# Kernel tuning notes

Measured on AMD Instinct MI355X. Metric: run time of the kernel, lower is better.

## Reference

```python
import jax, jax.numpy as jnp
import numpy as np

N_NODES = 8192
HIDDEN = 256
HEADS = 4
HEAD_DIM = HIDDEN // HEADS
NUM_EDGES = 4096
NUM_INC = 65536
LN_EPS = 1e-5


def setup_inputs() -> dict:
    key = jax.random.key(0)
    ks = jax.random.split(key, 8)
    scale = HIDDEN ** -0.5
    return {
        "x": jax.random.normal(ks[0], (N_NODES, HIDDEN), jnp.float32),
        "node_idx": jax.random.randint(ks[1], (NUM_INC,), 0, N_NODES),
        "edge_idx": jax.random.randint(ks[2], (NUM_INC,), 0, NUM_EDGES),
        "W_w": jax.random.normal(ks[3], (HIDDEN, HIDDEN), jnp.float32) * scale,
        "W_b": jax.random.normal(ks[4], (HIDDEN,), jnp.float32) * 0.02,
        "edge_att": jax.random.normal(ks[5], (HEADS, HEAD_DIM), jnp.float32) * scale,
        "out_w": jax.random.normal(ks[6], (HIDDEN, HIDDEN), jnp.float32) * scale,
        "out_b": jax.random.normal(ks[7], (HIDDEN,), jnp.float32) * 0.02,
    }


def reference(x, node_idx, edge_idx, W_w, W_b, edge_att, out_w, out_b):
    n = x.shape[0]
    e = node_idx.shape[0]
    # x' = W(x), split into heads: [N, heads, head_dim]
    xw = (x @ W_w.T + W_b).reshape(n, HEADS, HEAD_DIM)
    feat = xw[node_idx]                                   # [E, heads, hd]
    logits = jnp.einsum("ehd,hd->eh", feat, edge_att)      # [E, heads]
    # segment softmax over nodes within each hyperedge, per head
    seg_max = jax.ops.segment_max(logits, edge_idx, num_segments=NUM_EDGES)
    p = jnp.exp(logits - seg_max[edge_idx])
    seg_sum = jax.ops.segment_sum(p, edge_idx, num_segments=NUM_EDGES)
    attn = p / seg_sum[edge_idx]                           # [E, heads]
    attn_mean = attn.mean(axis=1)                          # mean over heads, [E]
    # hyperedges with < 2 nodes are skipped in the original
    sizes = jax.ops.segment_sum(jnp.ones((e,), x.dtype), edge_idx, num_segments=NUM_EDGES)
    valid = sizes[edge_idx] >= 2.0
    attn_mean = jnp.where(valid, attn_mean, 0.0)
    # scatter-add attention-weighted ORIGINAL features back to nodes
    contrib = attn_mean[:, None] * x[node_idx]             # [E, H]
    out = jnp.zeros_like(x).at[node_idx].add(contrib)
    # degree normalization counts ALL incidences (including size-1 edges)
    counts = jnp.zeros((n,), x.dtype).at[node_idx].add(1.0)
    out = out / jnp.clip(counts, 1.0)[:, None]
    out = out @ out_w.T + out_b
    # fresh nn.LayerNorm => affine identity, biased variance, eps=1e-5
    mu = out.mean(-1, keepdims=True)
    var = ((out - mu) ** 2).mean(-1, keepdims=True)
    out = (out - mu) / jnp.sqrt(var + LN_EPS)
    # NxN pairwise attention accumulation: AW[i,j] = sum_e attn_i(e)*count_j(e), diag zeroed
    A = jnp.zeros((n, NUM_EDGES), x.dtype).at[node_idx, edge_idx].add(attn_mean)
    B = jnp.zeros((n, NUM_EDGES), x.dtype).at[node_idx, edge_idx].add(1.0)
    attention_weights = A @ B.T
    attention_weights = attention_weights.at[jnp.diag_indices(n)].set(0.0)
    return out, attention_weights
```

## Files before the change

### kernel.cpp

```cpp
#include <hip/hip_runtime.h>
#include <stdint.h>

#define N_NODES  8192
#define HIDDEN   256
#define HEADS    4
#define HEAD_DIM 64
#define NUM_EDGES 4096
#define NUM_INC  65536
#define LN_EPS   1e-5f

typedef unsigned int uint_t;
typedef float __attribute__((ext_vector_type(4))) f4v;


#define OFF_SEGSZ    0
#define OFF_NCNT     16384
#define OFF_NFILL    49152
#define OFF_EFILL    81920
#define ZERO_BYTES   98304
#define OFF_VKH      98304
#define OFF_BL       102400
#define OFF_LOGIT    102464
#define OFF_NPTR     233536
#define OFF_EPTR     266320
#define OFF_SEGSUM   282720
#define OFF_NINC     348256
#define OFF_EMEM     610400
#define OFF_ITEM     872544

__global__ __launch_bounds__(256) void k_zero(uint_t* __restrict__ w) {
    w[blockIdx.x * 256 + threadIdx.x] = 0u;
}

__global__ __launch_bounds__(256) void k_fold(const float* __restrict__ Ww,
                                              const float* __restrict__ Wb,
                                              const float* __restrict__ ea,
                                              float* __restrict__ vkhT,
                                              float* __restrict__ bl) {
    int k = threadIdx.x, h = blockIdx.x;
    float a = 0.f;
    for (int d = 0; d < HEAD_DIM; ++d)
        a += ea[h * HEAD_DIM + d] * Ww[(size_t)(h * HEAD_DIM + d) * HIDDEN + k];
    vkhT[h * HIDDEN + k] = a;
    if (k == 0) {
        float b = 0.f;
        for (int d = 0; d < HEAD_DIM; ++d)
            b += Wb[h * HEAD_DIM + d] * ea[h * HEAD_DIM + d];
        bl[h] = b;
    }
}

__global__ __launch_bounds__(256) void k_logits(const float* __restrict__ x,
                                                const float* __restrict__ vkhT,
                                                const float* __restrict__ bl,
                                                float* __restrict__ logit) {
    __shared__ __align__(16) float xs[32 * HIDDEN];
    __shared__ __align__(16) float vs[HEADS * HIDDEN];
    __shared__ float bls[HEADS];
    int t = threadIdx.x, b = blockIdx.x;
    float4* xsv = (float4*)xs;
    const float4* xg = (const float4*)(x + (size_t)b * 32 * HIDDEN);
    #pragma unroll
    for (int i = 0; i < 8; ++i) xsv[i * 256 + t] = xg[i * 256 + t];
    ((float4*)vs)[t] = ((const float4*)vkhT)[t];
    if (t < HEADS) bls[t] = bl[t];
    __syncthreads();
    if (t < 128) {
        int n = t >> 2, h = t & 3;
        const float4* xr = (const float4*)(xs + n * HIDDEN);
        const float4* vr = (const float4*)(vs + h * HIDDEN);
        float acc = bls[h];
        for (int k4 = 0; k4 < HIDDEN / 4; ++k4) {
            float4 xv = xr[k4], vv = vr[k4];
            acc += xv.x * vv.x + xv.y * vv.y + xv.z * vv.z + xv.w * vv.w;
        }
        logit[(b * 32 + n) * HEADS + h] = acc;
    }
}

__global__ void k_pass1(const int* __restrict__ node_idx, const int* __restrict__ edge_idx,
                        int* __restrict__ seg_size, int* __restrict__ node_cnt) {
    int i = blockIdx.x * 256 + threadIdx.x;
    atomicAdd(&seg_size[edge_idx[i]], 1);
    atomicAdd(&node_cnt[node_idx[i]], 1);
}

__global__ __launch_bounds__(256) void k_scan(const int* __restrict__ node_cnt, int* __restrict__ node_ptr,
                                              const int* __restrict__ seg_size, int* __restrict__ edge_ptr) {
    __shared__ int part[256];
    const int* cnt; int* ptr; int n;
    if (blockIdx.x == 0) { cnt = node_cnt; ptr = node_ptr; n = N_NODES; }
    else                 { cnt = seg_size; ptr = edge_ptr; n = NUM_EDGES; }
    int t = threadIdx.x, C = n / 256;
    int s = 0;
    for (int j = 0; j < C; ++j) s += cnt[t * C + j];
    part[t] = s;
    __syncthreads();
    if (t == 0) {
        int run = 0;
        for (int i = 0; i < 256; ++i) { int tmp = part[i]; part[i] = run; run += tmp; }
        ptr[n] = run;
    }
    __syncthreads();
    int run = part[t];
    for (int j = 0; j < C; ++j) { ptr[t * C + j] = run; run += cnt[t * C + j]; }
}

__global__ void k_fill(const int* __restrict__ node_idx, const int* __restrict__ edge_idx,
                       const int* __restrict__ node_ptr, const int* __restrict__ edge_ptr,
                       int* __restrict__ node_fill, int* __restrict__ edge_fill,
                       int* __restrict__ node_inc, int* __restrict__ edge_mem) {
    int i = blockIdx.x * 256 + threadIdx.x;
    int n = node_idx[i], e = edge_idx[i];
    int p = node_ptr[n] + atomicAdd(&node_fill[n], 1);
    node_inc[p] = i;
    int q = edge_ptr[e] + atomicAdd(&edge_fill[e], 1);
    edge_mem[q] = n;
}

__global__ __launch_bounds__(256) void k_seg(const int* __restrict__ edge_ptr,
                                             const int* __restrict__ edge_mem,
                                             const float* __restrict__ logit,
                                             float* __restrict__ seg_sum) {
    int e = blockIdx.x * 256 + threadIdx.x;
    int qb = edge_ptr[e], qe = edge_ptr[e + 1];
    float s0 = 0, s1 = 0, s2 = 0, s3 = 0;
    for (int q = qb; q < qe; ++q) {
        int j = edge_mem[q];
        s0 += __expf(logit[j * 4 + 0]);
        s1 += __expf(logit[j * 4 + 1]);
        s2 += __expf(logit[j * 4 + 2]);
        s3 += __expf(logit[j * 4 + 3]);
    }
    seg_sum[e * 4 + 0] = s0; seg_sum[e * 4 + 1] = s1;
    seg_sum[e * 4 + 2] = s2; seg_sum[e * 4 + 3] = s3;
}

__global__ __launch_bounds__(256) void k_pairs(const int* __restrict__ node_inc,
                                               const int* __restrict__ node_idx,
                                               const int* __restrict__ edge_idx,
                                               const int* __restrict__ edge_ptr,
                                               const float* __restrict__ logit,
                                               const float* __restrict__ seg_sum,
                                               float4* __restrict__ item) {
    int p = blockIdx.x * 256 + threadIdx.x;
    int m = node_inc[p];
    int e = edge_idx[m];
    int qb = edge_ptr[e], qe = edge_ptr[e + 1];
    float a = 0.f;
    if (qe - qb >= 2) {
        int n = node_idx[m];
        float s = 0.f;
        #pragma unroll
        for (int h = 0; h < HEADS; ++h)
            s += __expf(logit[n * HEADS + h]) / seg_sum[e * HEADS + h];
        a = 0.25f * s;
    }
    float4 it;
    it.x = a;
    it.y = __int_as_float(qb);
    it.z = __int_as_float(qe);
    it.w = 0.f;
    item[p] = it;
}

__global__ __launch_bounds__(256) void k_out(const float* __restrict__ x,
                                             const int* __restrict__ node_ptr,
                                             const float4* __restrict__ item,
                                             const float* __restrict__ out_w,
                                             const float* __restrict__ out_b,
                                             float* __restrict__ out) {
    __shared__ __align__(16) float y[16][260];
    __shared__ float sr[16], mu_s[16], rs_s[16];
    int t = threadIdx.x;
    int R = blockIdx.x * 16;
    if (t < 16) {
        int n = R + t;
        int pb = node_ptr[n], pe = node_ptr[n + 1];
        float w = 0.f;
        for (int p = pb; p < pe; ++p) w += item[p].x;
        int c = pe - pb; if (c < 1) c = 1;
        sr[t] = w / (float)c;
    }
    __syncthreads();
    #pragma unroll
    for (int r = 0; r < 16; ++r)
        y[r][t] = sr[r] * x[(size_t)(R + r) * HIDDEN + t];
    __syncthreads();
    float acc[16];
    float bias = out_b[t];
    #pragma unroll
    for (int r = 0; r < 16; ++r) acc[r] = bias;
    const float4* wr4 = (const float4*)(out_w + (size_t)t * HIDDEN);
    for (int j4 = 0; j4 < HIDDEN / 4; ++j4) {
        float4 wv = wr4[j4];
        #pragma unroll
        for (int r = 0; r < 16; ++r) {
            float4 yv = *(const float4*)&y[r][j4 * 4];
            acc[r] += yv.x * wv.x + yv.y * wv.y + yv.z * wv.z + yv.w * wv.w;
        }
    }
    __syncthreads();
    #pragma unroll
    for (int r = 0; r < 16; ++r) y[r][t] = acc[r];
    __syncthreads();
    if (t < 16) {
        float m = 0.f;
        for (int j = 0; j < HIDDEN; ++j) m += y[t][j];
        m *= (1.0f / HIDDEN);
        float s2 = 0.f;
        for (int j = 0; j < HIDDEN; ++j) { float d = y[t][j] - m; s2 += d * d; }
        mu_s[t] = m;
        rs_s[t] = rsqrtf(s2 * (1.0f / HIDDEN) + LN_EPS);
    }
    __syncthreads();
    #pragma unroll
    for (int r = 0; r < 16; ++r)
        out[(size_t)(R + r) * HIDDEN + t] = (y[r][t] - mu_s[r]) * rs_s[r];
}

__global__ __launch_bounds__(256) void k_aw(const float4* __restrict__ item,
                                            const int* __restrict__ node_ptr,
                                            const int* __restrict__ edge_mem,
                                            float* __restrict__ AW) {
    __shared__ __align__(16) float row[N_NODES];
    int t = threadIdx.x, w = t >> 6, lane = t & 63;
    int i = blockIdx.x;
    float4* rowv = (float4*)row;
    #pragma unroll
    for (int c = 0; c < 8; ++c) rowv[c * 256 + t] = make_float4(0.f, 0.f, 0.f, 0.f);
    __syncthreads();
    int pb = node_ptr[i], pe = node_ptr[i + 1];
    for (int p = pb + w; p < pe; p += 4) {
        float4 it = item[p];
        float a = it.x;
        if (a != 0.f) {
            int qb = __float_as_int(it.y), qe = __float_as_int(it.z);
            for (int q = qb + lane; q < qe; q += 64)
                atomicAdd(&row[edge_mem[q]], a);
        }
    }
    __syncthreads();
    if (t == 0) row[i] = 0.f;
    __syncthreads();
    f4v* dst = (f4v*)(AW + (size_t)i * N_NODES);
    const f4v* src = (const f4v*)row;
    #pragma unroll
    for (int c = 0; c < 8; ++c)
        __builtin_nontemporal_store(src[c * 256 + t], &dst[c * 256 + t]);
}

extern "C" void kernel_launch(void* const* d_in, const int* in_sizes, int n_in,
                              void* d_out, int out_size, void* d_ws, size_t ws_size,
                              hipStream_t stream) {
    const float* x        = (const float*)d_in[0];
    const int*   node_idx = (const int*)d_in[1];
    const int*   edge_idx = (const int*)d_in[2];
    const float* Ww       = (const float*)d_in[3];
    const float* Wb       = (const float*)d_in[4];
    const float* ea       = (const float*)d_in[5];
    const float* ow       = (const float*)d_in[6];
    const float* ob       = (const float*)d_in[7];
    float* out0 = (float*)d_out;
    float* aw   = out0 + (size_t)N_NODES * HIDDEN;

    char* ws = (char*)d_ws;
    int*    seg_size  = (int*)(ws + OFF_SEGSZ);
    int*    node_cnt  = (int*)(ws + OFF_NCNT);
    int*    node_fill = (int*)(ws + OFF_NFILL);
    int*    edge_fill = (int*)(ws + OFF_EFILL);
    float*  vkhT      = (float*)(ws + OFF_VKH);
    float*  bl        = (float*)(ws + OFF_BL);
    float*  logit     = (float*)(ws + OFF_LOGIT);
    int*    node_ptr  = (int*)(ws + OFF_NPTR);
    int*    edge_ptr  = (int*)(ws + OFF_EPTR);
    float*  seg_sum   = (float*)(ws + OFF_SEGSUM);
    int*    node_inc  = (int*)(ws + OFF_NINC);
    int*    edge_mem  = (int*)(ws + OFF_EMEM);
    float4* item      = (float4*)(ws + OFF_ITEM);

    k_zero<<<ZERO_BYTES / 4 / 256, 256, 0, stream>>>((uint_t*)ws);
    k_fold<<<HEADS, 256, 0, stream>>>(Ww, Wb, ea, vkhT, bl);
    k_logits<<<N_NODES / 32, 256, 0, stream>>>(x, vkhT, bl, logit);
    k_pass1<<<NUM_INC / 256, 256, 0, stream>>>(node_idx, edge_idx, seg_size, node_cnt);
    k_scan<<<2, 256, 0, stream>>>(node_cnt, node_ptr, seg_size, edge_ptr);
    k_fill<<<NUM_INC / 256, 256, 0, stream>>>(node_idx, edge_idx, node_ptr, edge_ptr,
                                              node_fill, edge_fill, node_inc, edge_mem);
    k_seg<<<NUM_EDGES / 256, 256, 0, stream>>>(edge_ptr, edge_mem, logit, seg_sum);
    k_pairs<<<NUM_INC / 256, 256, 0, stream>>>(node_inc, node_idx, edge_idx, edge_ptr,
                                               logit, seg_sum, item);
    k_out<<<N_NODES / 16, 256, 0, stream>>>(x, node_ptr, item, ow, ob, out0);
    k_aw<<<N_NODES, 256, 0, stream>>>(item, node_ptr, edge_mem, aw);
}
```

Measured before the change: 397.1 us.

## Fuse zero/fold kernels and output projection into AW kernel, parallelize LayerNorm

Merges the workspace-zeroing and weight-folding kernels into one launch. It also folds the output projection plus LayerNorm into the first 512 blocks of the per-node AW kernel, reusing that kernel's shared buffer, which removes two launches. The LayerNorm statistics now come from wavefront shuffle reductions instead of 16 serial threads. The cost is that blocks 0-511 carry extra work, which could make them stragglers in the AW grid.

```diff
diff --git a/kernel.cpp b/kernel.cpp
--- a/kernel.cpp
+++ b/kernel.cpp
@@ -28,25 +28,26 @@
 #define OFF_EMEM     610400
 #define OFF_ITEM     872544
 
-__global__ __launch_bounds__(256) void k_zero(uint_t* __restrict__ w) {
-    w[blockIdx.x * 256 + threadIdx.x] = 0u;
-}
-
-__global__ __launch_bounds__(256) void k_fold(const float* __restrict__ Ww,
-                                              const float* __restrict__ Wb,
-                                              const float* __restrict__ ea,
-                                              float* __restrict__ vkhT,
-                                              float* __restrict__ bl) {
-    int k = threadIdx.x, h = blockIdx.x;
-    float a = 0.f;
-    for (int d = 0; d < HEAD_DIM; ++d)
-        a += ea[h * HEAD_DIM + d] * Ww[(size_t)(h * HEAD_DIM + d) * HIDDEN + k];
-    vkhT[h * HIDDEN + k] = a;
-    if (k == 0) {
-        float b = 0.f;
+__global__ __launch_bounds__(256) void k_foldzero(const float* __restrict__ Ww,
+                                                  const float* __restrict__ Wb,
+                                                  const float* __restrict__ ea,
+                                                  float* __restrict__ vkhT,
+                                                  float* __restrict__ bl,
+                                                  uint_t* __restrict__ zw) {
+    int t = threadIdx.x, b = blockIdx.x;
+    zw[b * 256 + t] = 0u;
+    if (b < HEADS) {
+        int k = t, h = b;
+        float a = 0.f;
         for (int d = 0; d < HEAD_DIM; ++d)
-            b += Wb[h * HEAD_DIM + d] * ea[h * HEAD_DIM + d];
-        bl[h] = b;
+            a += ea[h * HEAD_DIM + d] * Ww[(size_t)(h * HEAD_DIM + d) * HIDDEN + k];
+        vkhT[h * HIDDEN + k] = a;
+        if (k == 0) {
+            float s = 0.f;
+            for (int d = 0; d < HEAD_DIM; ++d)
+                s += Wb[h * HEAD_DIM + d] * ea[h * HEAD_DIM + d];
+            bl[h] = s;
+        }
     }
 }
 
@@ -164,23 +165,53 @@
     item[p] = it;
 }
 
-__global__ __launch_bounds__(256) void k_out(const float* __restrict__ x,
-                                             const int* __restrict__ node_ptr,
-                                             const float4* __restrict__ item,
-                                             const float* __restrict__ out_w,
-                                             const float* __restrict__ out_b,
-                                             float* __restrict__ out) {
-    __shared__ __align__(16) float y[16][260];
+__global__ __launch_bounds__(256) void k_aw_out(const float4* __restrict__ item,
+                                                const int* __restrict__ node_ptr,
+                                                const int* __restrict__ edge_mem,
+                                                const float* __restrict__ x,
+                                                const float* __restrict__ out_w,
+                                                const float* __restrict__ out_b,
+                                                float* __restrict__ AW,
+                                                float* __restrict__ out0) {
+    __shared__ __align__(16) float buf[N_NODES];
     __shared__ float sr[16], mu_s[16], rs_s[16];
-    int t = threadIdx.x;
-    int R = blockIdx.x * 16;
+    int t = threadIdx.x, w = t >> 6, lane = t & 63;
+    int i = blockIdx.x;
+
+    float4* rowv = (float4*)buf;
+    #pragma unroll
+    for (int c = 0; c < 8; ++c) rowv[c * 256 + t] = make_float4(0.f, 0.f, 0.f, 0.f);
+    __syncthreads();
+    int pb = node_ptr[i], pe = node_ptr[i + 1];
+    for (int p = pb + w; p < pe; p += 4) {
+        float4 it = item[p];
+        float a = it.x;
+        if (a != 0.f) {
+            int qb = __float_as_int(it.y), qe = __float_as_int(it.z);
+            for (int q = qb + lane; q < qe; q += 64)
+                atomicAdd(&buf[edge_mem[q]], a);
+        }
+    }
+    __syncthreads();
+    if (t == 0) buf[i] = 0.f;
+    __syncthreads();
+    f4v* dst = (f4v*)(AW + (size_t)i * N_NODES);
+    #pragma unroll
+    for (int c = 0; c < 8; ++c)
+        __builtin_nontemporal_store(((const f4v*)rowv)[c * 256 + t], &dst[c * 256 + t]);
+
+    if (i >= 512) return;
+
+    __syncthreads();
+    float (*y)[260] = (float (*)[260])buf;
+    int R = i * 16;
     if (t < 16) {
         int n = R + t;
-        int pb = node_ptr[n], pe = node_ptr[n + 1];
-        float w = 0.f;
-        for (int p = pb; p < pe; ++p) w += item[p].x;
-        int c = pe - pb; if (c < 1) c = 1;
-        sr[t] = w / (float)c;
+        int nb = node_ptr[n], ne = node_ptr[n + 1];
+        float ws = 0.f;
+        for (int p = nb; p < ne; ++p) ws += item[p].x;
+        int c = ne - nb; if (c < 1) c = 1;
+        sr[t] = ws / (float)c;
     }
     __syncthreads();
     #pragma unroll
@@ -204,50 +235,27 @@
     #pragma unroll
     for (int r = 0; r < 16; ++r) y[r][t] = acc[r];
     __syncthreads();
-    if (t < 16) {
-        float m = 0.f;
-        for (int j = 0; j < HIDDEN; ++j) m += y[t][j];
-        m *= (1.0f / HIDDEN);
-        float s2 = 0.f;
-        for (int j = 0; j < HIDDEN; ++j) { float d = y[t][j] - m; s2 += d * d; }
-        mu_s[t] = m;
-        rs_s[t] = rsqrtf(s2 * (1.0f / HIDDEN) + LN_EPS);
+    #pragma unroll
+    for (int rr = 0; rr < 4; ++rr) {
+        int r = (w << 2) | rr;
+        float v = y[r][lane] + y[r][lane + 64] + y[r][lane + 128] + y[r][lane + 192];
+        #pragma unroll
+        for (int off = 32; off; off >>= 1) v += __shfl_down(v, off, 64);
+        float mu = __shfl(v, 0, 64) * (1.0f / HIDDEN);
+        float d0 = y[r][lane] - mu, d1 = y[r][lane + 64] - mu;
+        float d2 = y[r][lane + 128] - mu, d3 = y[r][lane + 192] - mu;
+        float s2 = d0 * d0 + d1 * d1 + d2 * d2 + d3 * d3;
+        #pragma unroll
+        for (int off = 32; off; off >>= 1) s2 += __shfl_down(s2, off, 64);
+        if (lane == 0) {
+            mu_s[r] = mu;
+            rs_s[r] = rsqrtf(s2 * (1.0f / HIDDEN) + LN_EPS);
+        }
     }
     __syncthreads();
     #pragma unroll
     for (int r = 0; r < 16; ++r)
-        out[(size_t)(R + r) * HIDDEN + t] = (y[r][t] - mu_s[r]) * rs_s[r];
-}
-
-__global__ __launch_bounds__(256) void k_aw(const float4* __restrict__ item,
-                                            const int* __restrict__ node_ptr,
-                                            const int* __restrict__ edge_mem,
-                                            float* __restrict__ AW) {
-    __shared__ __align__(16) float row[N_NODES];
-    int t = threadIdx.x, w = t >> 6, lane = t & 63;
-    int i = blockIdx.x;
-    float4* rowv = (float4*)row;
-    #pragma unroll
-    for (int c = 0; c < 8; ++c) rowv[c * 256 + t] = make_float4(0.f, 0.f, 0.f, 0.f);
-    __syncthreads();
-    int pb = node_ptr[i], pe = node_ptr[i + 1];
-    for (int p = pb + w; p < pe; p += 4) {
-        float4 it = item[p];
-        float a = it.x;
-        if (a != 0.f) {
-            int qb = __float_as_int(it.y), qe = __float_as_int(it.z);
-            for (int q = qb + lane; q < qe; q += 64)
-                atomicAdd(&row[edge_mem[q]], a);
-        }
-    }
-    __syncthreads();
-    if (t == 0) row[i] = 0.f;
-    __syncthreads();
-    f4v* dst = (f4v*)(AW + (size_t)i * N_NODES);
-    const f4v* src = (const f4v*)row;
-    #pragma unroll
-    for (int c = 0; c < 8; ++c)
-        __builtin_nontemporal_store(src[c * 256 + t], &dst[c * 256 + t]);
+        out0[(size_t)(R + r) * HIDDEN + t] = (y[r][t] - mu_s[r]) * rs_s[r];
 }
 
 extern "C" void kernel_launch(void* const* d_in, const int* in_sizes, int n_in,
@@ -279,8 +287,7 @@
     int*    edge_mem  = (int*)(ws + OFF_EMEM);
     float4* item      = (float4*)(ws + OFF_ITEM);
 
-    k_zero<<<ZERO_BYTES / 4 / 256, 256, 0, stream>>>((uint_t*)ws);
-    k_fold<<<HEADS, 256, 0, stream>>>(Ww, Wb, ea, vkhT, bl);
+    k_foldzero<<<ZERO_BYTES / 4 / 256, 256, 0, stream>>>(Ww, Wb, ea, vkhT, bl, (uint_t*)ws);
     k_logits<<<N_NODES / 32, 256, 0, stream>>>(x, vkhT, bl, logit);
     k_pass1<<<NUM_INC / 256, 256, 0, stream>>>(node_idx, edge_idx, seg_size, node_cnt);
     k_scan<<<2, 256, 0, stream>>>(node_cnt, node_ptr, seg_size, edge_ptr);
@@ -289,6 +296,5 @@
     k_seg<<<NUM_EDGES / 256, 256, 0, stream>>>(edge_ptr, edge_mem, logit, seg_sum);
     k_pairs<<<NUM_INC / 256, 256, 0, stream>>>(node_inc, node_idx, edge_idx, edge_ptr,
                                                logit, seg_sum, item);
-    k_out<<<N_NODES / 16, 256, 0, stream>>>(x, node_ptr, item, ow, ob, out0);
-    k_aw<<<N_NODES, 256, 0, stream>>>(item, node_ptr, edge_mem, aw);
-}
+    k_aw_out<<<N_NODES, 256, 0, stream>>>(item, node_ptr, edge_mem, x, ow, ob, aw, out0);
+}
```

Measured after the change: 368.3 us. 7.3% less time.
